# Kernel optimization log

Hardware: AMD Instinct MI355X
Metric: run time of the kernel (lower is better)

The kernel has to match this reference:

```python
import jax, jax.numpy as jnp
import numpy as np
import math

D_MODEL = 512
NUM_HEADS = 8
D_K = D_MODEL // NUM_HEADS
MAX_LEN = 500
BATCH = 32
SEQ = 480


def setup_inputs() -> dict:
    key = jax.random.key(0)
    ks = jax.random.split(key, 10)
    s = 0.02
    x = jax.random.normal(ks[0], (BATCH, SEQ, D_MODEL), dtype=jnp.float32)
    wq = jax.random.normal(ks[1], (D_MODEL, D_MODEL), dtype=jnp.float32) * s
    bq = jnp.zeros((D_MODEL,), jnp.float32)
    wk = jax.random.normal(ks[2], (D_MODEL, D_MODEL), dtype=jnp.float32) * s
    bk = jnp.zeros((D_MODEL,), jnp.float32)
    wv = jax.random.normal(ks[3], (D_MODEL, D_MODEL), dtype=jnp.float32) * s
    bv = jnp.zeros((D_MODEL,), jnp.float32)
    wo = jax.random.normal(ks[4], (D_MODEL, D_MODEL), dtype=jnp.float32) * s
    bo = jnp.zeros((D_MODEL,), jnp.float32)
    rel_bias = jax.random.normal(ks[5], (NUM_HEADS, MAX_LEN, MAX_LEN), dtype=jnp.float32) * 0.02
    return {"x": x, "wq": wq, "bq": bq, "wk": wk, "bk": bk, "wv": wv,
            "bv": bv, "wo": wo, "bo": bo, "rel_bias": rel_bias}


def reference(x, wq, bq, wk, bk, wv, bv, wo, bo, rel_bias):
    B, S, D = x.shape
    H, dk = NUM_HEADS, D_K
    scale = math.sqrt(dk)
    # QKV projections -> [B, H, S, dk]
    q = (x @ wq + bq).reshape(B, S, H, dk).transpose(0, 2, 1, 3)
    k = (x @ wk + bk).reshape(B, S, H, dk).transpose(0, 2, 1, 3)
    v = (x @ wv + bv).reshape(B, S, H, dk).transpose(0, 2, 1, 3)
    scores = jnp.einsum('bhqd,bhkd->bhqk', q, k) / scale
    scores = scores + rel_bias[None, :, :S, :S]
    causal = jnp.triu(jnp.ones((S, S), dtype=bool), k=1)  # True where j > i
    scores = jnp.where(causal[None, None], -jnp.inf, scores)
    attn = jax.nn.softmax(scores, axis=-1)
    ctx = jnp.einsum('bhqk,bhkd->bhqd', attn, v)
    ctx = ctx.transpose(0, 2, 1, 3).reshape(B, S, D)
    out = ctx @ wo + bo
    return out, attn.mean(axis=1)
```

## Files before the change

### kernel.cpp

```cpp
#include <hip/hip_runtime.h>
#include <hip/hip_bf16.h>


typedef unsigned short ushort_t;
typedef __attribute__((ext_vector_type(8))) short short8;
typedef __attribute__((ext_vector_type(4))) float floatx4;
typedef __attribute__((ext_vector_type(2))) __fp16 half2v;

#define NB 32
#define NS 480
#define ND 512
#define NH 8
#define NDK 64
#define MAXLEN 500
#define PSTR 36
#define SCL 0.18033688f

__device__ __forceinline__ ushort_t f2bf(float f) {
  union { float f; unsigned u; } v; v.f = f;
  unsigned r = v.u + 0x7FFFu + ((v.u >> 16) & 1u);
  return (ushort_t)(r >> 16);
}

#define GLOAD_LDS16(g, l)                                                      \
  __builtin_amdgcn_global_load_lds(                                            \
      (const __attribute__((address_space(1))) void*)(g),                      \
      (__attribute__((address_space(3))) void*)(l), 16, 0, 0)

__global__ __launch_bounds__(256)
void cvt_xw(const float* __restrict__ x, const float* __restrict__ wq,
            const float* __restrict__ wk, const float* __restrict__ wv,
            const float* __restrict__ wo, ushort_t* __restrict__ xb,
            ushort_t* __restrict__ wqT, ushort_t* __restrict__ wkT,
            ushort_t* __restrict__ wvT, ushort_t* __restrict__ woT) {
  __shared__ float t[32][33];
  const int bid = blockIdx.x;
  if (bid < 7680) {
    int idx = bid * 256 + threadIdx.x;
    float4 v = ((const float4*)x)[idx];
    ushort4 o;
    o.x = f2bf(v.x); o.y = f2bf(v.y); o.z = f2bf(v.z); o.w = f2bf(v.w);
    ((ushort4*)xb)[idx] = o;
    return;
  }
  const int q = bid - 7680;
  const int z = q >> 8;
  const float* w = (z == 0) ? wq : (z == 1) ? wk : (z == 2) ? wv : wo;
  ushort_t* wT = (z == 0) ? wqT : (z == 1) ? wkT : (z == 2) ? wvT : woT;
  int k0 = (q & 15) * 32, n0 = ((q >> 4) & 15) * 32;
  int tx = threadIdx.x & 31, ty = threadIdx.x >> 5;
#pragma unroll
  for (int yy = 0; yy < 4; ++yy)
    t[ty + yy * 8][tx] = w[(k0 + ty + yy * 8) * ND + n0 + tx];
  __syncthreads();
#pragma unroll
  for (int yy = 0; yy < 4; ++yy)
    wT[(n0 + ty + yy * 8) * ND + k0 + tx] = f2bf(t[tx][ty + yy * 8]);
}

__global__ void cvt_rbt(const float* __restrict__ rel_bias, float* __restrict__ rbt) {
  int kt = blockIdx.x, ib = blockIdx.y, h = blockIdx.z;
  int lm = threadIdx.x & 15, ii = threadIdx.x >> 4;
  int i = ib * 16 + ii;
  float f0 = rel_bias[((size_t)h * MAXLEN + i) * MAXLEN + kt * 32 + lm] * 1.44269504f;
  float f1 = rel_bias[((size_t)h * MAXLEN + i) * MAXLEN + kt * 32 + 16 + lm] * 1.44269504f;
  float2 o = {f0, f1};
  *(float2*)&rbt[(((size_t)h * 15 + kt) * NS + i) * 32 + 2 * lm] = o;
}

__global__ __launch_bounds__(256)
void qkv_gemm(const ushort_t* __restrict__ xb,
              const ushort_t* __restrict__ wqT, const ushort_t* __restrict__ wkT,
              const ushort_t* __restrict__ wvT,
              const float* __restrict__ bq, const float* __restrict__ bk,
              const float* __restrict__ bv,
              ushort_t* __restrict__ qb, ushort_t* __restrict__ kb,
              ushort_t* __restrict__ vtil) {
  __shared__ __align__(16) ushort_t sA[2][128 * 64];
  __shared__ __align__(16) ushort_t sB[2][128 * 64];
  const int tid = threadIdx.x;
  const int wid = tid >> 6, lane = tid & 63;
  const int lm = lane & 15, quad = lane >> 4;
  const int wr = wid >> 1, wc = wid & 1;
  const int z = blockIdx.z;

  floatx4 zero4 = {0.f, 0.f, 0.f, 0.f};
  floatx4 acc[4][4];
#pragma unroll
  for (int i = 0; i < 4; ++i)
#pragma unroll
    for (int j = 0; j < 4; ++j) acc[i][j] = zero4;

  const int srow_ = tid >> 3, skc = tid & 7;
  const int skcs = skc ^ (srow_ & 7);

  if (z < 2) {
    if (blockIdx.x >= 120) return;
    const int row0 = blockIdx.x * 128;
    const int col0 = blockIdx.y * 128;
    const ushort_t* Bt = (z == 0) ? wqT : wkT;
    const float* bias = (z == 0) ? bq : bk;

#pragma unroll
    for (int c = 0; c < 4; ++c) {
      int row = c * 32 + srow_;
      GLOAD_LDS16(xb + (row0 + row) * ND + skcs * 8, &sA[0][(c * 256 + wid * 64) * 8]);
      GLOAD_LDS16(Bt + (col0 + row) * ND + skcs * 8, &sB[0][(c * 256 + wid * 64) * 8]);
    }
    __syncthreads();

    int buf = 0;
    for (int t = 0; t < 8; ++t) {
      if (t < 7) {
        int k0n = (t + 1) * 64;
#pragma unroll
        for (int c = 0; c < 4; ++c) {
          int row = c * 32 + srow_;
          GLOAD_LDS16(xb + (row0 + row) * ND + k0n + skcs * 8,
                      &sA[buf ^ 1][(c * 256 + wid * 64) * 8]);
          GLOAD_LDS16(Bt + (col0 + row) * ND + k0n + skcs * 8,
                      &sB[buf ^ 1][(c * 256 + wid * 64) * 8]);
        }
      }
#pragma unroll
      for (int h2 = 0; h2 < 2; ++h2) {
        short8 a[4], b[4];
#pragma unroll
        for (int i = 0; i < 4; ++i) {
          int row = wr * 64 + i * 16 + lm;
          a[i] = *(const short8*)&sA[buf][row * 64 + (((h2 << 2) | quad) ^ (lm & 7)) * 8];
        }
#pragma unroll
        for (int j = 0; j < 4; ++j) {
          int row = wc * 64 + j * 16 + lm;
          b[j] = *(const short8*)&sB[buf][row * 64 + (((h2 << 2) | quad) ^ (lm & 7)) * 8];
        }
#pragma unroll
        for (int i = 0; i < 4; ++i)
#pragma unroll
          for (int j = 0; j < 4; ++j)
            acc[i][j] = __builtin_amdgcn_mfma_f32_16x16x32_bf16(a[i], b[j], acc[i][j], 0, 0, 0);
      }
      __syncthreads();
      buf ^= 1;
    }

    float bsv[4];
#pragma unroll
    for (int j = 0; j < 4; ++j) bsv[j] = bias[col0 + wc * 64 + j * 16 + lm];

#pragma unroll
    for (int i = 0; i < 4; ++i)
#pragma unroll
      for (int j = 0; j < 4; ++j)
#pragma unroll
        for (int r = 0; r < 4; ++r) {
          int m = row0 + wr * 64 + i * 16 + quad * 4 + r;
          int n = col0 + wc * 64 + j * 16 + lm;
          float val = acc[i][j][r] + bsv[j];
          int bb = m / NS, s = m - bb * NS;
          int h = n >> 6, d = n & 63;
          ushort_t o = f2bf(val);
          if (z == 0) qb[((bb * NH + h) * NS + s) * NDK + d] = o;
          else        kb[((bb * NH + h) * NS + s) * NDK + d] = o;
        }
  } else {
    const int b = blockIdx.x >> 2;
    const int row0 = (blockIdx.x & 3) * 128;
    const int col0 = blockIdx.y * 128;
    const ushort_t* xbb = xb + (size_t)b * NS * ND;

#pragma unroll
    for (int c = 0; c < 4; ++c) {
      int row = c * 32 + srow_;
      GLOAD_LDS16(wvT + (row0 + row) * ND + skcs * 8, &sA[0][(c * 256 + wid * 64) * 8]);
      int sr = min(col0 + row, NS - 1);
      GLOAD_LDS16(xbb + sr * ND + skcs * 8, &sB[0][(c * 256 + wid * 64) * 8]);
    }
    __syncthreads();

    int buf = 0;
    for (int t = 0; t < 8; ++t) {
      if (t < 7) {
        int k0n = (t + 1) * 64;
#pragma unroll
        for (int c = 0; c < 4; ++c) {
          int row = c * 32 + srow_;
          GLOAD_LDS16(wvT + (row0 + row) * ND + k0n + skcs * 8,
                      &sA[buf ^ 1][(c * 256 + wid * 64) * 8]);
          int sr = min(col0 + row, NS - 1);
          GLOAD_LDS16(xbb + sr * ND + k0n + skcs * 8,
                      &sB[buf ^ 1][(c * 256 + wid * 64) * 8]);
        }
      }
#pragma unroll
      for (int h2 = 0; h2 < 2; ++h2) {
        short8 a[4], b2[4];
#pragma unroll
        for (int i = 0; i < 4; ++i) {
          int row = wr * 64 + i * 16 + lm;
          a[i] = *(const short8*)&sA[buf][row * 64 + (((h2 << 2) | quad) ^ (lm & 7)) * 8];
        }
#pragma unroll
        for (int j = 0; j < 4; ++j) {
          int row = wc * 64 + j * 16 + lm;
          b2[j] = *(const short8*)&sB[buf][row * 64 + (((h2 << 2) | quad) ^ (lm & 7)) * 8];
        }
#pragma unroll
        for (int i = 0; i < 4; ++i)
#pragma unroll
          for (int j = 0; j < 4; ++j)
            acc[i][j] = __builtin_amdgcn_mfma_f32_16x16x32_bf16(a[i], b2[j], acc[i][j], 0, 0, 0);
      }
      __syncthreads();
      buf ^= 1;
    }

#pragma unroll
    for (int i = 0; i < 4; ++i)
#pragma unroll
      for (int r = 0; r < 4; ++r) {
        int m = row0 + wr * 64 + i * 16 + quad * 4 + r;
        float bias = bv[m];
#pragma unroll
        for (int j = 0; j < 4; ++j) {
          int n = col0 + wc * 64 + j * 16 + lm;
          if (n < NS) {
            size_t idx = (((size_t)b * NH + (m >> 6)) * 15 + (n >> 5)) * 2048 +
                         (m & 63) * 32 + (n & 31);
            vtil[idx] = f2bf(acc[i][j][r] + bias);
          }
        }
      }
  }
}

__global__ __launch_bounds__(256)
void flash_attn(const ushort_t* __restrict__ qb, const ushort_t* __restrict__ kb,
                const ushort_t* __restrict__ vtil, const float* __restrict__ rbt,
                ushort_t* __restrict__ ctxb, float* __restrict__ cst,
                uint4* __restrict__ pscr) {
  const int bh = blockIdx.x;
  const int b = bh >> 3, h = bh & 7;
  const int tid = threadIdx.x;
  const int wid = tid >> 6, lane = tid & 63;
  const int lm = lane & 15, quad = lane >> 4;

  __shared__ __align__(16) ushort_t sP[4][32 * PSTR];

  const int slot = blockIdx.y * 4 + wid;
  const int tA = (slot == 7) ? 14 : slot;
  const int tB = (slot == 7) ? -1 : 13 - slot;

  const ushort_t* qh = qb + (size_t)bh * NS * NDK;
  const ushort_t* kh = kb + (size_t)bh * NS * NDK;
  const ushort_t* vb = vtil + (size_t)bh * 15 * 2048;
  const float* rb = rbt + (size_t)h * 15 * NS * 32;

#pragma unroll 1
  for (int ti = 0; ti < 2; ++ti) {
    const int t = (ti == 0) ? tA : tB;
    if (t < 0) break;
    const int nkt = t + 1;
    uint4* pp = pscr + ((size_t)(bh * 120 + (t * (t + 1)) / 2)) * 128 + lane;

    short8 aq[2][2];
#pragma unroll
    for (int g = 0; g < 2; ++g) {
      aq[g][0] = *(const short8*)&qh[(t * 32 + g * 16 + lm) * NDK + quad * 8];
      aq[g][1] = *(const short8*)&qh[(t * 32 + g * 16 + lm) * NDK + 32 + quad * 8];
    }

    float lsum[2][4];
    floatx4 O[2][4];
    floatx4 zero4 = {0.f, 0.f, 0.f, 0.f};
#pragma unroll
    for (int g = 0; g < 2; ++g) {
#pragma unroll
      for (int r = 0; r < 4; ++r) lsum[g][r] = 0.f;
#pragma unroll
      for (int jd = 0; jd < 4; ++jd) O[g][jd] = zero4;
    }

    for (int kt = 0; kt < nkt; ++kt) {
      const int kvA = kt * 32 + lm;
      const int kvB = kvA + 16;
      short8 bkA0 = *(const short8*)&kh[kvA * NDK + quad * 8];
      short8 bkA1 = *(const short8*)&kh[kvA * NDK + 32 + quad * 8];
      short8 bkB0 = *(const short8*)&kh[kvB * NDK + quad * 8];
      short8 bkB1 = *(const short8*)&kh[kvB * NDK + 32 + quad * 8];
      short8 bv2[4];
#pragma unroll
      for (int jd = 0; jd < 4; ++jd)
        bv2[jd] = *(const short8*)&vb[kt * 2048 + (jd * 16 + lm) * 32 + quad * 8];
      float2 bb[2][4];
#pragma unroll
      for (int g = 0; g < 2; ++g)
#pragma unroll
        for (int r = 0; r < 4; ++r) {
          int i = t * 32 + g * 16 + quad * 4 + r;
          bb[g][r] = *(const float2*)&rb[((size_t)kt * NS + i) * 32 + 2 * lm];
        }

      floatx4 sA[2], sB[2];
      __builtin_amdgcn_s_setprio(1);
#pragma unroll
      for (int g = 0; g < 2; ++g) {
        floatx4 s = zero4;
        s = __builtin_amdgcn_mfma_f32_16x16x32_bf16(aq[g][0], bkA0, s, 0, 0, 0);
        s = __builtin_amdgcn_mfma_f32_16x16x32_bf16(aq[g][1], bkA1, s, 0, 0, 0);
        sA[g] = s;
        s = zero4;
        s = __builtin_amdgcn_mfma_f32_16x16x32_bf16(aq[g][0], bkB0, s, 0, 0, 0);
        s = __builtin_amdgcn_mfma_f32_16x16x32_bf16(aq[g][1], bkB1, s, 0, 0, 0);
        sB[g] = s;
      }
      __builtin_amdgcn_s_setprio(0);

      const bool diag = (kt == t);
#pragma unroll
      for (int g = 0; g < 2; ++g) {
        unsigned pw[4];
#pragma unroll
        for (int r = 0; r < 4; ++r) {
          float p0 = __builtin_amdgcn_exp2f(fmaf(sA[g][r], SCL, bb[g][r].x));
          float p1 = __builtin_amdgcn_exp2f(fmaf(sB[g][r], SCL, bb[g][r].y));
          if (diag) {
            int i = t * 32 + g * 16 + quad * 4 + r;
            if (kvA > i) p0 = 0.f;
            if (kvB > i) p1 = 0.f;
          }
          lsum[g][r] += p0 + p1;
          unsigned pk;
          asm("v_cvt_pk_bf16_f32 %0, %1, %2" : "=v"(pk) : "v"(p0), "v"(p1));
          sP[wid][(g * 16 + quad * 4 + r) * PSTR + lm] = (ushort_t)(pk & 0xffffu);
          sP[wid][(g * 16 + quad * 4 + r) * PSTR + 16 + lm] = (ushort_t)(pk >> 16);
          half2v hp = __builtin_amdgcn_cvt_pkrtz(p0, p1);
          pw[r] = *(unsigned*)&hp;
        }
        uint4 pq = {pw[0], pw[1], pw[2], pw[3]};
        pp[(size_t)kt * 128 + g * 64] = pq;
      }

      __builtin_amdgcn_s_setprio(1);
#pragma unroll
      for (int g = 0; g < 2; ++g) {
        short8 ap = *(const short8*)&sP[wid][(g * 16 + lm) * PSTR + quad * 8];
#pragma unroll
        for (int jd = 0; jd < 4; ++jd)
          O[g][jd] = __builtin_amdgcn_mfma_f32_16x16x32_bf16(ap, bv2[jd], O[g][jd], 0, 0, 0);
      }
      __builtin_amdgcn_s_setprio(0);
    }

#pragma unroll
    for (int off = 1; off < 16; off <<= 1)
#pragma unroll
      for (int g = 0; g < 2; ++g)
#pragma unroll
        for (int r = 0; r < 4; ++r) lsum[g][r] += __shfl_xor(lsum[g][r], off, 64);

#pragma unroll
    for (int g = 0; g < 2; ++g) {
      float rinv[4];
#pragma unroll
      for (int r = 0; r < 4; ++r) rinv[r] = 1.f / lsum[g][r];
#pragma unroll
      for (int jd = 0; jd < 4; ++jd)
#pragma unroll
        for (int r = 0; r < 4; ++r) {
          int i = t * 32 + g * 16 + quad * 4 + r;
          ctxb[((size_t)b * NS + i) * ND + h * NDK + jd * 16 + lm] =
              f2bf(O[g][jd][r] * rinv[r]);
        }
      if (lm == 0) {
#pragma unroll
        for (int r = 0; r < 4; ++r) {
          int i = t * 32 + g * 16 + quad * 4 + r;
          cst[(size_t)bh * NS + i] = rinv[r];
        }
      }
    }
  }
}

__global__ __launch_bounds__(64)
void attn_mean_p(const uint4* __restrict__ pscr, const float* __restrict__ cst,
                 float* __restrict__ am) {
  const int b = blockIdx.x, t = blockIdx.y, kt = blockIdx.z;
  const int lane = threadIdx.x;
  const int lm = lane & 15, quad = lane >> 4;
  float* outp = am + ((size_t)b * NS + t * 32) * NS + (size_t)kt * 32;
  if (kt > t) {
#pragma unroll
    for (int g = 0; g < 2; ++g)
#pragma unroll
      for (int r = 0; r < 4; ++r) {
        int row = g * 16 + quad * 4 + r;
        outp[(size_t)row * NS + lm] = 0.f;
        outp[(size_t)row * NS + 16 + lm] = 0.f;
      }
    return;
  }
  const int m = (t * (t + 1)) / 2 + kt;
  float a0[2][4], a1[2][4];
#pragma unroll
  for (int g = 0; g < 2; ++g)
#pragma unroll
    for (int r = 0; r < 4; ++r) { a0[g][r] = 0.f; a1[g][r] = 0.f; }

#pragma unroll
  for (int h = 0; h < NH; ++h) {
    const uint4* pp = pscr + ((size_t)(b * NH + h) * 120 + m) * 128 + lane;
    uint4 q0 = pp[0];
    uint4 q1 = pp[64];
    unsigned pu[8] = {q0.x, q0.y, q0.z, q0.w, q1.x, q1.y, q1.z, q1.w};
    const float* cp = cst + (size_t)(b * NH + h) * NS + t * 32 + quad * 4;
    float4 rv0 = *(const float4*)cp;
    float4 rv1 = *(const float4*)(cp + 16);
    float rv[8] = {rv0.x, rv0.y, rv0.z, rv0.w, rv1.x, rv1.y, rv1.z, rv1.w};
#pragma unroll
    for (int g = 0; g < 2; ++g)
#pragma unroll
      for (int r = 0; r < 4; ++r) {
        half2v hp = *(half2v*)&pu[g * 4 + r];
        a0[g][r] = fmaf((float)hp.x, rv[g * 4 + r], a0[g][r]);
        a1[g][r] = fmaf((float)hp.y, rv[g * 4 + r], a1[g][r]);
      }
  }

#pragma unroll
  for (int g = 0; g < 2; ++g)
#pragma unroll
    for (int r = 0; r < 4; ++r) {
      int row = g * 16 + quad * 4 + r;
      outp[(size_t)row * NS + lm] = a0[g][r] * 0.125f;
      outp[(size_t)row * NS + 16 + lm] = a1[g][r] * 0.125f;
    }
}

__global__ __launch_bounds__(256)
void out_gemm(const ushort_t* __restrict__ ctxb, const ushort_t* __restrict__ woT,
              const float* __restrict__ bo, float* __restrict__ out) {
  __shared__ __align__(16) ushort_t sA[2][128 * 64];
  __shared__ __align__(16) ushort_t sB[2][128 * 64];
  const int tid = threadIdx.x;
  const int wid = tid >> 6, lane = tid & 63;
  const int lm = lane & 15, quad = lane >> 4;
  const int wr = wid >> 1, wc = wid & 1;
  const int row0 = blockIdx.x * 128;
  const int col0 = blockIdx.y * 128;
  const int srow_ = tid >> 3, skc = tid & 7;
  const int skcs = skc ^ (srow_ & 7);

  floatx4 zero4 = {0.f, 0.f, 0.f, 0.f};
  floatx4 acc[4][4];
#pragma unroll
  for (int i = 0; i < 4; ++i)
#pragma unroll
    for (int j = 0; j < 4; ++j) acc[i][j] = zero4;

#pragma unroll
  for (int c = 0; c < 4; ++c) {
    int row = c * 32 + srow_;
    GLOAD_LDS16(ctxb + (row0 + row) * ND + skcs * 8, &sA[0][(c * 256 + wid * 64) * 8]);
    GLOAD_LDS16(woT + (col0 + row) * ND + skcs * 8, &sB[0][(c * 256 + wid * 64) * 8]);
  }
  __syncthreads();

  int buf = 0;
  for (int t = 0; t < 8; ++t) {
    if (t < 7) {
      int k0n = (t + 1) * 64;
#pragma unroll
      for (int c = 0; c < 4; ++c) {
        int row = c * 32 + srow_;
        GLOAD_LDS16(ctxb + (row0 + row) * ND + k0n + skcs * 8,
                    &sA[buf ^ 1][(c * 256 + wid * 64) * 8]);
        GLOAD_LDS16(woT + (col0 + row) * ND + k0n + skcs * 8,
                    &sB[buf ^ 1][(c * 256 + wid * 64) * 8]);
      }
    }
#pragma unroll
    for (int h2 = 0; h2 < 2; ++h2) {
      short8 a[4], b[4];
#pragma unroll
      for (int i = 0; i < 4; ++i) {
        int row = wr * 64 + i * 16 + lm;
        a[i] = *(const short8*)&sA[buf][row * 64 + (((h2 << 2) | quad) ^ (lm & 7)) * 8];
      }
#pragma unroll
      for (int j = 0; j < 4; ++j) {
        int row = wc * 64 + j * 16 + lm;
        b[j] = *(const short8*)&sB[buf][row * 64 + (((h2 << 2) | quad) ^ (lm & 7)) * 8];
      }
#pragma unroll
      for (int i = 0; i < 4; ++i)
#pragma unroll
        for (int j = 0; j < 4; ++j)
          acc[i][j] = __builtin_amdgcn_mfma_f32_16x16x32_bf16(a[i], b[j], acc[i][j], 0, 0, 0);
    }
    __syncthreads();
    buf ^= 1;
  }

  float bsv[4];
#pragma unroll
  for (int j = 0; j < 4; ++j) bsv[j] = bo[col0 + wc * 64 + j * 16 + lm];

#pragma unroll
  for (int i = 0; i < 4; ++i)
#pragma unroll
    for (int j = 0; j < 4; ++j)
#pragma unroll
      for (int r = 0; r < 4; ++r) {
        int m = row0 + wr * 64 + i * 16 + quad * 4 + r;
        int n = col0 + wc * 64 + j * 16 + lm;
        out[m * ND + n] = acc[i][j][r] + bsv[j];
      }
}

extern "C" void kernel_launch(void* const* d_in, const int* in_sizes, int n_in,
                              void* d_out, int out_size, void* d_ws, size_t ws_size,
                              hipStream_t stream) {
  const float* x  = (const float*)d_in[0];
  const float* wq = (const float*)d_in[1];
  const float* bq = (const float*)d_in[2];
  const float* wk = (const float*)d_in[3];
  const float* bk = (const float*)d_in[4];
  const float* wv = (const float*)d_in[5];
  const float* bv = (const float*)d_in[6];
  const float* wo = (const float*)d_in[7];
  const float* bo = (const float*)d_in[8];
  const float* rel_bias = (const float*)d_in[9];

  char* w = (char*)d_ws;
  ushort_t* xb  = (ushort_t*)w;
  ushort_t* wqT = (ushort_t*)(w + 15728640);
  ushort_t* wkT = wqT + 262144;
  ushort_t* wvT = wkT + 262144;
  ushort_t* woT = wvT + 262144;
  ushort_t* qb  = (ushort_t*)(w + 15728640 + 4 * 524288);
  ushort_t* kb  = qb + 7864320;
  ushort_t* vtil = kb + 7864320;
  ushort_t* ctxb = vtil + 7864320;
  float* cstat = (float*)(w + 80740352);
  uint4* pscr = (uint4*)(w + 81264640);
  float* rbt = (float*)w;

  float* out0 = (float*)d_out;
  float* attn_mean = out0 + 7864320;

  cvt_xw<<<dim3(8704), dim3(256), 0, stream>>>(x, wq, wk, wv, wo, xb, wqT, wkT, wvT, woT);
  qkv_gemm<<<dim3(128, 4, 3), dim3(256), 0, stream>>>(xb, wqT, wkT, wvT, bq, bk, bv,
                                                      qb, kb, vtil);
  cvt_rbt<<<dim3(15, 30, 8), dim3(256), 0, stream>>>(rel_bias, rbt);
  flash_attn<<<dim3(256, 2), dim3(256), 0, stream>>>(qb, kb, vtil, rbt, ctxb, cstat, pscr);
  attn_mean_p<<<dim3(32, 15, 15), dim3(64), 0, stream>>>(pscr, cstat, attn_mean);
  out_gemm<<<dim3(120, 4), dim3(256), 0, stream>>>(ctxb, woT, bo, out0);
}
```

Baseline: 220.9 us.

## Split flash-attention KV loop across two waves per query tile with LDS merge

Each query-tile slot is now handled by a 128-thread block of two waves instead of one wave. The waves interleave the KV tiles (even and odd) and combine their partial O accumulators and row sums through shared memory before the final normalisation and store. The goal is to halve the serial KV-loop length per wave and double the number of waves in flight, improving latency hiding and load balance on the causal triangle. In exchange it adds an LDS round trip, two block barriers per tile, and one idle wave during the epilogue.

After: 225.7 us. +2.2%, slower.

```diff
diff --git a/kernel.cpp b/kernel.cpp
--- a/kernel.cpp
+++ b/kernel.cpp
@@ -235,7 +235,7 @@
   }
 }
 
-__global__ __launch_bounds__(256)
+__global__ __launch_bounds__(128)
 void flash_attn(const ushort_t* __restrict__ qb, const ushort_t* __restrict__ kb,
                 const ushort_t* __restrict__ vtil, const float* __restrict__ rbt,
                 ushort_t* __restrict__ ctxb, float* __restrict__ cst,
@@ -246,9 +246,11 @@
   const int wid = tid >> 6, lane = tid & 63;
   const int lm = lane & 15, quad = lane >> 4;
 
-  __shared__ __align__(16) ushort_t sP[4][32 * PSTR];
-
-  const int slot = blockIdx.y * 4 + wid;
+  __shared__ __align__(16) ushort_t sP[2][32 * PSTR];
+  __shared__ float mO[64][33];
+  __shared__ float mL[64][9];
+
+  const int slot = blockIdx.y;
   const int tA = (slot == 7) ? 14 : slot;
   const int tB = (slot == 7) ? -1 : 13 - slot;
 
@@ -282,7 +284,7 @@
       for (int jd = 0; jd < 4; ++jd) O[g][jd] = zero4;
     }
 
-    for (int kt = 0; kt < nkt; ++kt) {
+    for (int kt = wid; kt < nkt; kt += 2) {
       const int kvA = kt * 32 + lm;
       const int kvB = kvA + 16;
       short8 bkA0 = *(const short8*)&kh[kvA * NDK + quad * 8];
@@ -353,34 +355,61 @@
       __builtin_amdgcn_s_setprio(0);
     }
 
-#pragma unroll
-    for (int off = 1; off < 16; off <<= 1)
-#pragma unroll
-      for (int g = 0; g < 2; ++g)
-#pragma unroll
-        for (int r = 0; r < 4; ++r) lsum[g][r] += __shfl_xor(lsum[g][r], off, 64);
-
-#pragma unroll
-    for (int g = 0; g < 2; ++g) {
-      float rinv[4];
-#pragma unroll
-      for (int r = 0; r < 4; ++r) rinv[r] = 1.f / lsum[g][r];
-#pragma unroll
-      for (int jd = 0; jd < 4; ++jd)
-#pragma unroll
-        for (int r = 0; r < 4; ++r) {
-          int i = t * 32 + g * 16 + quad * 4 + r;
-          ctxb[((size_t)b * NS + i) * ND + h * NDK + jd * 16 + lm] =
-              f2bf(O[g][jd][r] * rinv[r]);
-        }
-      if (lm == 0) {
-#pragma unroll
-        for (int r = 0; r < 4; ++r) {
-          int i = t * 32 + g * 16 + quad * 4 + r;
-          cst[(size_t)bh * NS + i] = rinv[r];
-        }
-      }
-    }
+    if (wid == 1) {
+#pragma unroll
+      for (int g = 0; g < 2; ++g) {
+#pragma unroll
+        for (int r = 0; r < 4; ++r) mL[lane][g * 4 + r] = lsum[g][r];
+#pragma unroll
+        for (int jd = 0; jd < 4; ++jd)
+#pragma unroll
+          for (int r = 0; r < 4; ++r)
+            mO[lane][(g * 4 + jd) * 4 + r] = O[g][jd][r];
+      }
+    }
+    __syncthreads();
+    if (wid == 0) {
+#pragma unroll
+      for (int g = 0; g < 2; ++g) {
+#pragma unroll
+        for (int r = 0; r < 4; ++r) lsum[g][r] += mL[lane][g * 4 + r];
+#pragma unroll
+        for (int jd = 0; jd < 4; ++jd)
+#pragma unroll
+          for (int r = 0; r < 4; ++r)
+            O[g][jd][r] += mO[lane][(g * 4 + jd) * 4 + r];
+      }
+
+#pragma unroll
+      for (int off = 1; off < 16; off <<= 1)
+#pragma unroll
+        for (int g = 0; g < 2; ++g)
+#pragma unroll
+          for (int r = 0; r < 4; ++r) lsum[g][r] += __shfl_xor(lsum[g][r], off, 64);
+
+#pragma unroll
+      for (int g = 0; g < 2; ++g) {
+        float rinv[4];
+#pragma unroll
+        for (int r = 0; r < 4; ++r) rinv[r] = 1.f / lsum[g][r];
+#pragma unroll
+        for (int jd = 0; jd < 4; ++jd)
+#pragma unroll
+          for (int r = 0; r < 4; ++r) {
+            int i = t * 32 + g * 16 + quad * 4 + r;
+            ctxb[((size_t)b * NS + i) * ND + h * NDK + jd * 16 + lm] =
+                f2bf(O[g][jd][r] * rinv[r]);
+          }
+        if (lm == 0) {
+#pragma unroll
+          for (int r = 0; r < 4; ++r) {
+            int i = t * 32 + g * 16 + quad * 4 + r;
+            cst[(size_t)bh * NS + i] = rinv[r];
+          }
+        }
+      }
+    }
+    __syncthreads();
   }
 }
 
@@ -555,7 +584,7 @@
   qkv_gemm<<<dim3(128, 4, 3), dim3(256), 0, stream>>>(xb, wqT, wkT, wvT, bq, bk, bv,
                                                       qb, kb, vtil);
   cvt_rbt<<<dim3(15, 30, 8), dim3(256), 0, stream>>>(rel_bias, rbt);
-  flash_attn<<<dim3(256, 2), dim3(256), 0, stream>>>(qb, kb, vtil, rbt, ctxb, cstat, pscr);
+  flash_attn<<<dim3(256, 8), dim3(128), 0, stream>>>(qb, kb, vtil, rbt, ctxb, cstat, pscr);
   attn_mean_p<<<dim3(32, 15, 15), dim3(64), 0, stream>>>(pscr, cstat, attn_mean);
   out_gemm<<<dim3(120, 4), dim3(256), 0, stream>>>(ctxb, woT, bo, out0);
 }
```
